# Kernel optimization log

Measured on AMD Instinct MI355X. Metric: run time of the kernel, lower is better.

## Reference

```python
import jax, jax.numpy as jnp
import numpy as np

B_, L, DM = 4, 1024, 1024
DI, DS, DR, DC = 1024, 16, 64, 4
NH = 4
DK = DM // NH


def setup_inputs() -> dict:
    key = jax.random.key(0)
    ks = jax.random.split(key, 16)
    def w(i, shape, scale=0.02):
        return jax.random.normal(ks[i], shape, dtype=jnp.float32) * scale
    inp = {
        "x": jax.random.normal(ks[0], (B_, L, DM), dtype=jnp.float32),
        "xx": jax.random.normal(ks[1], (B_, L, DI), dtype=jnp.float32),
        "in_proj_w": w(2, (DI, DM)),
        "conv_w": w(3, (DI, 1, DC)),            # depthwise conv, groups=DI
        "conv_b": jnp.zeros((DI,), jnp.float32),
        "x_proj_w": w(4, (DR + 2 * DS, DI)),
        "dt_proj_w": w(5, (DI, DR)),
        "dt_proj_b": jnp.zeros((DI,), jnp.float32),
        "A_log": jnp.log(jnp.tile(jnp.arange(1, DS + 1, dtype=jnp.float32)[None, :], (DI, 1))),
        "D": jnp.ones((DI,), jnp.float32),
        "wq": w(6, (DM, DM)), "bq": jnp.zeros((DM,), jnp.float32),
        "wk": w(7, (DM, DM)), "bk": jnp.zeros((DM,), jnp.float32),
        "wv": w(8, (DM, DM)), "bv": jnp.zeros((DM,), jnp.float32),
        "wo": w(9, (DM, DM)), "bo": jnp.zeros((DM,), jnp.float32),
    }
    return inp


def _stim_forward(x, xx, in_proj_w, conv_w, conv_b, x_proj_w, dt_proj_w, dt_proj_b,
                  A_log, D, wq, bq, wk, bk, wv, bv, wo, bo):
    b, l, _ = xx.shape
    # query branch: in_proj (Linear, no bias)
    q = x @ in_proj_w.T                                    # (b, l, DI)
    # kv branch: causal depthwise conv1d (padding d_conv-1, truncated to l)
    xc = jnp.transpose(xx, (0, 2, 1))                      # (b, DI, l)
    xc = jax.lax.conv_general_dilated(
        xc, conv_w, window_strides=(1,), padding=[(DC - 1, 0)],
        dimension_numbers=("NCH", "OIH", "NCH"), feature_group_count=DI)
    xc = xc + conv_b[None, :, None]
    u = jax.nn.silu(jnp.transpose(xc, (0, 2, 1)))          # (b, l, DI)
    # SSM parameter projections
    A = -jnp.exp(A_log)                                    # (DI, DS)
    x_dbl = u @ x_proj_w.T                                 # (b, l, DR+2*DS)
    delta, Bm, Cm = jnp.split(x_dbl, [DR, DR + DS], axis=-1)
    delta = jax.nn.softplus(delta @ dt_proj_w.T + dt_proj_b)  # (b, l, DI)
    deltaA = jnp.exp(jnp.einsum("bld,dn->bldn", delta, A))    # (b, l, DI, DS)
    deltaBu = jnp.einsum("bld,bln,bld->bldn", delta, Bm, u)   # (b, l, DI, DS)
    # selective scan over time
    def step(h, inp):
        dA_t, dBu_t, C_t = inp
        h = dA_t * h + dBu_t                               # (b, DI, DS)
        y_t = jnp.einsum("bdn,bn->bd", h, C_t)             # (b, DI)
        return h, y_t
    h0 = jnp.zeros((b, DI, DS), dtype=u.dtype)
    _, ys = jax.lax.scan(step, h0, (jnp.moveaxis(deltaA, 1, 0),
                                    jnp.moveaxis(deltaBu, 1, 0),
                                    jnp.moveaxis(Cm, 1, 0)))
    y = jnp.moveaxis(ys, 0, 1) + u * D                     # (b, l, DI)
    # cross attention: query = q, key/value = y
    Q = (q @ wq.T + bq).reshape(b, l, NH, DK).transpose(0, 2, 1, 3)
    K = (y @ wk.T + bk).reshape(b, l, NH, DK).transpose(0, 2, 1, 3)
    V = (y @ wv.T + bv).reshape(b, l, NH, DK).transpose(0, 2, 1, 3)
    scale = 1.0 / np.sqrt(DK).astype(np.float32)
    scores = jnp.einsum("bhqd,bhkd->bhqk", Q, K) * scale
    attn = jax.nn.softmax(scores, axis=-1)
    out = jnp.einsum("bhqk,bhkd->bhqd", attn, V)
    out = out.transpose(0, 2, 1, 3).reshape(b, l, DM)
    return out @ wo.T + bo


def reference(x, xx, in_proj_w, conv_w, conv_b, x_proj_w, dt_proj_w, dt_proj_b,
              A_log, D, wq, bq, wk, bk, wv, bv, wo, bo):
    return _stim_forward(x, xx, in_proj_w, conv_w, conv_b, x_proj_w, dt_proj_w,
                         dt_proj_b, A_log, D, wq, bq, wk, bk, wv, bv, wo, bo)
```

## Files before the change

kernel.cpp:

```cpp
#include <hip/hip_runtime.h>
#include <math.h>

#define B_  4
#define L_  1024
#define DM  1024
#define DI  1024
#define DS  16
#define DR  64
#define DCV 4
#define NH  4
#define DK  256

#define NCH 32
#define CHL (L_ / NCH)

typedef __attribute__((ext_vector_type(8))) short short8;
typedef __attribute__((ext_vector_type(4))) float floatx4;

static __device__ __forceinline__ unsigned short f2bf(float f) {
    unsigned int u = __float_as_uint(f);
    u += 0x7fffu + ((u >> 16) & 1u);
    return (unsigned short)(u >> 16);
}
static __device__ __forceinline__ float bf2f(unsigned short s) {
    return __uint_as_float(((unsigned int)s) << 16);
}

struct CastArgs {
    const float* s[8];
    unsigned short* d[8];
    int n[8];
    int ns[8];
};

__global__ __launch_bounds__(256) void cast_multi(CastArgs ca)
{
    int y = blockIdx.y;
    int i = (blockIdx.x * 256 + threadIdx.x) * 4;
    if (i >= ca.n[y]) return;
    const float* s = ca.s[y];
    unsigned short* d = ca.d[y];
    int ns = ca.ns[y];
    ushort4 o;
    if (i + 4 <= ns) {
        float4 v = *(const float4*)(s + i);
        o.x = f2bf(v.x); o.y = f2bf(v.y); o.z = f2bf(v.z); o.w = f2bf(v.w);
    } else {
        float v[4];
#pragma unroll
        for (int j = 0; j < 4; j++) v[j] = (i + j < ns) ? s[i + j] : 0.f;
        o.x = f2bf(v[0]); o.y = f2bf(v[1]); o.z = f2bf(v[2]); o.w = f2bf(v[3]);
    }
    *(ushort4*)(d + i) = o;
}

struct GDesc {
    const unsigned short* A;
    const unsigned short* W;
    const float* bias;
    float* Cf;
    unsigned short* Cb;
    int K, lda, ldw, ldc, ldc2;
    int mode;
    float scale;
    int gx, gy;
};
struct GArgs { GDesc g[3]; };

__global__ __launch_bounds__(256) void gemm_multi(GArgs ga)
{
    GDesc g = ga.g[blockIdx.z];
    if ((int)blockIdx.x >= g.gx || (int)blockIdx.y >= g.gy) return;

    __shared__ __align__(16) unsigned short Asm[128 * 32];
    __shared__ __align__(16) unsigned short Bsm[128 * 32];

    int tid = threadIdx.x;
    int wid = tid >> 6;
    int lane = tid & 63;
    int wm = wid & 1, wn = wid >> 1;
    int lr = lane & 15, quad = lane >> 4;

    const unsigned short* Ab = g.A + (size_t)blockIdx.y * 128 * g.lda;
    const unsigned short* Wb = g.W + (size_t)blockIdx.x * 128 * g.ldw;

    int srow = tid >> 2;
    int scol = (tid & 3) * 8;
    const unsigned short* Ap = Ab + (size_t)srow * g.lda + scol;
    const unsigned short* Wp = Wb + (size_t)srow * g.ldw + scol;

    unsigned short* lA0 = &Asm[(wid * 16) * 32];
    unsigned short* lA1 = &Asm[(64 + wid * 16) * 32];
    unsigned short* lB0 = &Bsm[(wid * 16) * 32];
    unsigned short* lB1 = &Bsm[(64 + wid * 16) * 32];

    floatx4 acc[4][4];
#pragma unroll
    for (int i = 0; i < 4; i++)
#pragma unroll
        for (int j = 0; j < 4; j++) acc[i][j] = (floatx4){0.f, 0.f, 0.f, 0.f};

#define GLL(gp, lp) __builtin_amdgcn_global_load_lds( \
        (const __attribute__((address_space(1))) void*)(gp), \
        (__attribute__((address_space(3))) void*)(lp), 16, 0, 0)

    for (int k0 = 0; k0 < g.K; k0 += 32) {
        GLL(Ap, lA0);
        GLL(Ap + (size_t)64 * g.lda, lA1);
        GLL(Wp, lB0);
        GLL(Wp + (size_t)64 * g.ldw, lB1);
        Ap += 32; Wp += 32;
        __syncthreads();

        short8 af[4], bf[4];
#pragma unroll
        for (int mt = 0; mt < 4; mt++)
            af[mt] = *(const short8*)&Asm[(wm * 64 + mt * 16 + lr) * 32 + quad * 8];
#pragma unroll
        for (int nt = 0; nt < 4; nt++)
            bf[nt] = *(const short8*)&Bsm[(wn * 64 + nt * 16 + lr) * 32 + quad * 8];
#pragma unroll
        for (int mt = 0; mt < 4; mt++)
#pragma unroll
            for (int nt = 0; nt < 4; nt++)
                acc[mt][nt] = __builtin_amdgcn_mfma_f32_16x16x32_bf16(
                    af[mt], bf[nt], acc[mt][nt], 0, 0, 0);
        __syncthreads();
    }
#undef GLL

    int bm = blockIdx.y * 128, bn = blockIdx.x * 128;
    int m = g.mode & 3;
#pragma unroll
    for (int mt = 0; mt < 4; mt++) {
#pragma unroll
        for (int nt = 0; nt < 4; nt++) {
            int row0 = bm + wm * 64 + mt * 16 + quad * 4;
            int col = bn + wn * 64 + nt * 16 + lr;
            float bv = g.bias ? g.bias[col] : 0.f;
#pragma unroll
            for (int i = 0; i < 4; i++) {
                float v = acc[mt][nt][i] * g.scale + bv;
                if (g.mode & 4) v = (v > 15.f) ? v : log1pf(__expf(v));
                if (m == 0) {
                    g.Cf[(size_t)(row0 + i) * g.ldc + col] = v;
                } else if (m == 1) {
                    g.Cb[(size_t)(row0 + i) * g.ldc + col] = f2bf(v);
                } else {
                    g.Cf[(size_t)(row0 + i) * g.ldc + col] = v;
                    g.Cb[(size_t)(row0 + i) * g.ldc2 + col] = f2bf(v);
                }
            }
        }
    }
}

__global__ __launch_bounds__(256) void flash_attn(
    const unsigned short* __restrict__ Q, const unsigned short* __restrict__ Kg,
    const unsigned short* __restrict__ VT, unsigned short* __restrict__ O)
{
    __shared__ __align__(16) unsigned short Ks[64 * 264];
    __shared__ __align__(16) unsigned short Pp[4 * 16 * 72];

    int bh = blockIdx.y;
    int b = bh >> 2, h = bh & 3;
    int q0 = blockIdx.x * 64;
    int tid = threadIdx.x;
    int wid = tid >> 6, lane = tid & 63;
    int lr = lane & 15, quad = lane >> 4;
    const float scale = 0.0625f;

    short8 qf[8];
    const unsigned short* qbase = Q + ((size_t)(b * L_ + q0 + wid * 16 + lr)) * 1024 + h * DK;
#pragma unroll
    for (int kf = 0; kf < 8; kf++)
        qf[kf] = *(const short8*)(qbase + kf * 32 + quad * 8);

    floatx4 o_acc[16];
#pragma unroll
    for (int i = 0; i < 16; i++) o_acc[i] = (floatx4){0.f, 0.f, 0.f, 0.f};
    float m_i[4] = {-3e38f, -3e38f, -3e38f, -3e38f};
    float l_i[4] = {0.f, 0.f, 0.f, 0.f};

    int srow = tid >> 5;
    int sc16 = tid & 31;
    unsigned short* pw = &Pp[wid * 16 * 72];

    for (int kt = 0; kt < 16; kt++) {
        int k0 = kt * 64;
        __syncthreads();
        {
            const unsigned short* kb = Kg + ((size_t)(b * L_ + k0 + srow)) * 1024 + h * DK + sc16 * 8;
            unsigned short* kd = &Ks[srow * 264 + sc16 * 8];
#pragma unroll
            for (int rd = 0; rd < 8; rd++)
                *(short8*)(kd + rd * 8 * 264) = *(const short8*)(kb + (size_t)rd * 8 * 1024);
        }
        __syncthreads();

        floatx4 sacc[4];
#pragma unroll
        for (int nt = 0; nt < 4; nt++) sacc[nt] = (floatx4){0.f, 0.f, 0.f, 0.f};
#pragma unroll
        for (int kf = 0; kf < 8; kf++) {
#pragma unroll
            for (int nt = 0; nt < 4; nt++) {
                short8 kfr = *(const short8*)&Ks[(nt * 16 + lr) * 264 + kf * 32 + quad * 8];
                sacc[nt] = __builtin_amdgcn_mfma_f32_16x16x32_bf16(qf[kf], kfr, sacc[nt], 0, 0, 0);
            }
        }

        float p_[4][4];
        float al[4];
#pragma unroll
        for (int i = 0; i < 4; i++) {
            float tm = sacc[0][i];
            tm = fmaxf(tm, sacc[1][i]);
            tm = fmaxf(tm, sacc[2][i]);
            tm = fmaxf(tm, sacc[3][i]);
            tm *= scale;
            tm = fmaxf(tm, __shfl_xor(tm, 1));
            tm = fmaxf(tm, __shfl_xor(tm, 2));
            tm = fmaxf(tm, __shfl_xor(tm, 4));
            tm = fmaxf(tm, __shfl_xor(tm, 8));
            float mn = fmaxf(m_i[i], tm);
            al[i] = __expf(m_i[i] - mn);
            m_i[i] = mn;
            float ts = 0.f;
#pragma unroll
            for (int nt = 0; nt < 4; nt++) {
                float pv = __expf(sacc[nt][i] * scale - mn);
                p_[nt][i] = pv;
                ts += pv;
            }
            ts += __shfl_xor(ts, 1);
            ts += __shfl_xor(ts, 2);
            ts += __shfl_xor(ts, 4);
            ts += __shfl_xor(ts, 8);
            l_i[i] = al[i] * l_i[i] + ts;
        }

#pragma unroll
        for (int nt = 0; nt < 4; nt++)
#pragma unroll
            for (int i = 0; i < 4; i++)
                pw[(quad * 4 + i) * 72 + nt * 16 + lr] = f2bf(p_[nt][i]);

#pragma unroll
        for (int ntd = 0; ntd < 16; ntd++) {
            floatx4 t = o_acc[ntd];
            t[0] *= al[0]; t[1] *= al[1]; t[2] *= al[2]; t[3] *= al[3];
            o_acc[ntd] = t;
        }

        const unsigned short* vb = VT + ((size_t)bh * DK + lr) * 1024 + k0 + quad * 8;
#pragma unroll
        for (int ko = 0; ko < 2; ko++) {
            short8 pf = *(const short8*)&pw[lr * 72 + ko * 32 + quad * 8];
#pragma unroll
            for (int ntd = 0; ntd < 16; ntd++) {
                short8 vf = *(const short8*)(vb + (size_t)ntd * 16 * 1024 + ko * 32);
                o_acc[ntd] = __builtin_amdgcn_mfma_f32_16x16x32_bf16(pf, vf, o_acc[ntd], 0, 0, 0);
            }
        }
    }

    float inv[4];
#pragma unroll
    for (int i = 0; i < 4; i++) inv[i] = 1.0f / l_i[i];
    unsigned short* ob = O + ((size_t)(b * L_ + q0 + wid * 16 + quad * 4)) * 1024 + h * DK + lr;
#pragma unroll
    for (int ntd = 0; ntd < 16; ntd++)
#pragma unroll
        for (int i = 0; i < 4; i++)
            ob[(size_t)i * 1024 + ntd * 16] = f2bf(o_acc[ntd][i] * inv[i]);
}

__global__ __launch_bounds__(256) void conv_silu_kernel(
    const float* __restrict__ xx, const float* __restrict__ cw,
    const float* __restrict__ cb, float* __restrict__ u,
    unsigned short* __restrict__ ub)
{
    int idx = blockIdx.x * 256 + threadIdx.x;
    int d = idx & (DI - 1);
    int l = (idx >> 10) & (L_ - 1);
    int b = idx >> 20;
    const float* xb = xx + (size_t)b * L_ * DI + d;
    float z = cb[d];
#pragma unroll
    for (int j = 0; j < DCV; j++) {
        int t = l - (DCV - 1) + j;
        if (t >= 0) z += xb[(size_t)t * DI] * cw[d * DCV + j];
    }
    float v = z / (1.0f + __expf(-z));
    u[idx] = v;
    ub[idx] = f2bf(v);
}

__global__ __launch_bounds__(256) void scan_a(
    const float* __restrict__ delta, const float* __restrict__ u,
    const float* __restrict__ xdbl, const float* __restrict__ A_log,
    float* __restrict__ Hc, float* __restrict__ sumdv)
{
    int gid = blockIdx.x * 256 + threadIdx.x;
    int c = gid >> 12;
    int bd = gid & 4095;
    int b = bd >> 10, d = bd & 1023;

    float a[16];
#pragma unroll
    for (int j = 0; j < 4; j++) {
        float4 al = *(const float4*)(A_log + d * 16 + j * 4);
        a[j * 4 + 0] = -__expf(al.x); a[j * 4 + 1] = -__expf(al.y);
        a[j * 4 + 2] = -__expf(al.z); a[j * 4 + 3] = -__expf(al.w);
    }
    float h[16];
#pragma unroll
    for (int n = 0; n < 16; n++) h[n] = 0.f;
    float sd = 0.f;

    int t0 = c * CHL;
    const float* dp = delta + ((size_t)(b * L_) + t0) * DI + d;
    const float* up = u + ((size_t)(b * L_) + t0) * DI + d;
    const float* xp = xdbl + ((size_t)(b * L_) + t0) * 128;

#pragma unroll 4
    for (int t = 0; t < CHL; t++) {
        float dv = dp[t * DI];
        float uv = up[t * DI];
        float duv = dv * uv;
        sd += dv;
        float Bv[16];
#pragma unroll
        for (int j = 0; j < 4; j++) {
            float4 bq = *(const float4*)(xp + t * 128 + 64 + j * 4);
            Bv[j * 4 + 0] = bq.x; Bv[j * 4 + 1] = bq.y;
            Bv[j * 4 + 2] = bq.z; Bv[j * 4 + 3] = bq.w;
        }
#pragma unroll
        for (int n = 0; n < 16; n++)
            h[n] = __expf(dv * a[n]) * h[n] + duv * Bv[n];
    }

    float* hp = Hc + ((size_t)c * 4096 + bd) * 16;
#pragma unroll
    for (int j = 0; j < 4; j++)
        *(float4*)(hp + j * 4) = make_float4(h[j * 4], h[j * 4 + 1], h[j * 4 + 2], h[j * 4 + 3]);
    sumdv[c * 4096 + bd] = sd;
}

__global__ __launch_bounds__(256) void scan_b(
    float* __restrict__ Hc, const float* __restrict__ sumdv,
    const float* __restrict__ A_log)
{
    int bd = blockIdx.x * 256 + threadIdx.x;
    int d = bd & 1023;

    float a[16];
#pragma unroll
    for (int j = 0; j < 4; j++) {
        float4 al = *(const float4*)(A_log + d * 16 + j * 4);
        a[j * 4 + 0] = -__expf(al.x); a[j * 4 + 1] = -__expf(al.y);
        a[j * 4 + 2] = -__expf(al.z); a[j * 4 + 3] = -__expf(al.w);
    }
    float H[16];
#pragma unroll
    for (int n = 0; n < 16; n++) H[n] = 0.f;

    for (int c = 0; c < NCH; c++) {
        float* hp = Hc + ((size_t)c * 4096 + bd) * 16;
        float sdv = sumdv[c * 4096 + bd];
        float hc[16];
#pragma unroll
        for (int j = 0; j < 4; j++) {
            float4 q = *(const float4*)(hp + j * 4);
            hc[j * 4 + 0] = q.x; hc[j * 4 + 1] = q.y; hc[j * 4 + 2] = q.z; hc[j * 4 + 3] = q.w;
        }
#pragma unroll
        for (int j = 0; j < 4; j++)
            *(float4*)(hp + j * 4) = make_float4(H[j * 4], H[j * 4 + 1], H[j * 4 + 2], H[j * 4 + 3]);
#pragma unroll
        for (int n = 0; n < 16; n++)
            H[n] = __expf(a[n] * sdv) * H[n] + hc[n];
    }
}

__global__ __launch_bounds__(256) void scan_c(
    const float* __restrict__ delta, const float* __restrict__ u,
    const float* __restrict__ xdbl, const float* __restrict__ A_log,
    const float* __restrict__ Dv, const float* __restrict__ Hstart,
    unsigned short* __restrict__ y)
{
    int gid = blockIdx.x * 256 + threadIdx.x;
    int c = gid >> 12;
    int bd = gid & 4095;
    int b = bd >> 10, d = bd & 1023;

    float a[16];
#pragma unroll
    for (int j = 0; j < 4; j++) {
        float4 al = *(const float4*)(A_log + d * 16 + j * 4);
        a[j * 4 + 0] = -__expf(al.x); a[j * 4 + 1] = -__expf(al.y);
        a[j * 4 + 2] = -__expf(al.z); a[j * 4 + 3] = -__expf(al.w);
    }
    float h[16];
    const float* hp = Hstart + ((size_t)c * 4096 + bd) * 16;
#pragma unroll
    for (int j = 0; j < 4; j++) {
        float4 q = *(const float4*)(hp + j * 4);
        h[j * 4 + 0] = q.x; h[j * 4 + 1] = q.y; h[j * 4 + 2] = q.z; h[j * 4 + 3] = q.w;
    }
    float Dd = Dv[d];

    int t0 = c * CHL;
    const float* dp = delta + ((size_t)(b * L_) + t0) * DI + d;
    const float* up = u + ((size_t)(b * L_) + t0) * DI + d;
    const float* xp = xdbl + ((size_t)(b * L_) + t0) * 128;
    unsigned short* yp = y + ((size_t)(b * L_) + t0) * DI + d;

#pragma unroll 4
    for (int t = 0; t < CHL; t++) {
        float dv = dp[t * DI];
        float uv = up[t * DI];
        float duv = dv * uv;
        float Bv[16], Cv[16];
#pragma unroll
        for (int j = 0; j < 4; j++) {
            float4 bq = *(const float4*)(xp + t * 128 + 64 + j * 4);
            Bv[j * 4 + 0] = bq.x; Bv[j * 4 + 1] = bq.y;
            Bv[j * 4 + 2] = bq.z; Bv[j * 4 + 3] = bq.w;
            float4 cq = *(const float4*)(xp + t * 128 + 80 + j * 4);
            Cv[j * 4 + 0] = cq.x; Cv[j * 4 + 1] = cq.y;
            Cv[j * 4 + 2] = cq.z; Cv[j * 4 + 3] = cq.w;
        }
        float ys = 0.f;
#pragma unroll
        for (int n = 0; n < 16; n++) {
            h[n] = __expf(dv * a[n]) * h[n] + duv * Bv[n];
            ys += h[n] * Cv[n];
        }
        yp[t * DI] = f2bf(ys + uv * Dd);
    }
}

__global__ __launch_bounds__(256) void transpose_v(
    const unsigned short* __restrict__ V, unsigned short* __restrict__ VT)
{
    __shared__ unsigned short tl[32][36];
    int bh = blockIdx.z;
    int b = bh >> 2, h = bh & 3;
    int l0 = blockIdx.x * 32, d0 = blockIdx.y * 32;
    int tid = threadIdx.x;
    int r = tid >> 3, c4 = (tid & 7) * 4;

    const unsigned short* src = V + ((size_t)(b * L_ + l0 + r)) * 1024 + h * DK + d0 + c4;
    ushort4 v = *(const ushort4*)src;
    tl[r][c4 + 0] = v.x; tl[r][c4 + 1] = v.y; tl[r][c4 + 2] = v.z; tl[r][c4 + 3] = v.w;
    __syncthreads();

    unsigned short* dst = VT + ((size_t)bh * DK + d0 + r) * L_ + l0 + c4;
    ushort4 o;
    o.x = tl[c4 + 0][r]; o.y = tl[c4 + 1][r]; o.z = tl[c4 + 2][r]; o.w = tl[c4 + 3][r];
    *(ushort4*)dst = o;
}

extern "C" void kernel_launch(void* const* d_in, const int* in_sizes, int n_in,
                              void* d_out, int out_size, void* d_ws, size_t ws_size,
                              hipStream_t stream)
{
    const float* x         = (const float*)d_in[0];
    const float* xx        = (const float*)d_in[1];
    const float* in_proj_w = (const float*)d_in[2];
    const float* conv_w    = (const float*)d_in[3];
    const float* conv_b    = (const float*)d_in[4];
    const float* x_proj_w  = (const float*)d_in[5];
    const float* dt_proj_w = (const float*)d_in[6];
    const float* dt_proj_b = (const float*)d_in[7];
    const float* A_log     = (const float*)d_in[8];
    const float* Dvec      = (const float*)d_in[9];
    const float* wq        = (const float*)d_in[10];
    const float* bq        = (const float*)d_in[11];
    const float* wk        = (const float*)d_in[12];
    const float* bk        = (const float*)d_in[13];
    const float* wv        = (const float*)d_in[14];
    const float* bv        = (const float*)d_in[15];
    const float* wo        = (const float*)d_in[16];
    const float* bo        = (const float*)d_in[17];
    float* out = (float*)d_out;

    char* w = (char*)d_ws;
    const size_t MB = 1024 * 1024, KB = 1024;
    float*          u_f    = (float*)(w + 0);
    float*          delta  = (float*)(w + 16 * MB);
    unsigned short* x_bf   = (unsigned short*)(w + 32 * MB);
    unsigned short* Q_bf   = x_bf;
    unsigned short* q_bf   = (unsigned short*)(w + 40 * MB);
    unsigned short* VT     = q_bf;
    unsigned short* y_bf   = (unsigned short*)(w + 48 * MB);
    unsigned short* AO     = y_bf;
    unsigned short* K_bf   = (unsigned short*)(w + 56 * MB);
    unsigned short* V_bf   = (unsigned short*)(w + 64 * MB);
    unsigned short* u_bf   = (unsigned short*)(w + 72 * MB);
    float*          Hc     = (float*)(w + 72 * MB);
    float*          xdbl   = (float*)(w + 80 * MB);
    unsigned short* xdblb  = (unsigned short*)(w + 82 * MB);
    unsigned short* w_in   = (unsigned short*)(w + 83 * MB);
    unsigned short* w_q    = (unsigned short*)(w + 85 * MB);
    unsigned short* w_k    = (unsigned short*)(w + 87 * MB);
    unsigned short* w_v    = (unsigned short*)(w + 89 * MB);
    unsigned short* w_o    = (unsigned short*)(w + 91 * MB);
    unsigned short* w_xp   = (unsigned short*)(w + 93 * MB);
    unsigned short* w_dt   = (unsigned short*)(w + 93 * MB + 256 * KB);
    float*          sumdv  = (float*)(w + 93 * MB + 384 * KB);

    dim3 blk(256);

    CastArgs ca;
    ca.s[0] = x;         ca.d[0] = x_bf;  ca.n[0] = 4194304; ca.ns[0] = 4194304;
    ca.s[1] = in_proj_w; ca.d[1] = w_in;  ca.n[1] = 1048576; ca.ns[1] = 1048576;
    ca.s[2] = wq;        ca.d[2] = w_q;   ca.n[2] = 1048576; ca.ns[2] = 1048576;
    ca.s[3] = wk;        ca.d[3] = w_k;   ca.n[3] = 1048576; ca.ns[3] = 1048576;
    ca.s[4] = wv;        ca.d[4] = w_v;   ca.n[4] = 1048576; ca.ns[4] = 1048576;
    ca.s[5] = wo;        ca.d[5] = w_o;   ca.n[5] = 1048576; ca.ns[5] = 1048576;
    ca.s[6] = x_proj_w;  ca.d[6] = w_xp;  ca.n[6] = 131072;  ca.ns[6] = 98304;
    ca.s[7] = dt_proj_w; ca.d[7] = w_dt;  ca.n[7] = 65536;   ca.ns[7] = 65536;
    cast_multi<<<dim3(4096, 8), blk, 0, stream>>>(ca);

    conv_silu_kernel<<<dim3(16384), blk, 0, stream>>>(xx, conv_w, conv_b, u_f, u_bf);

    {
        GArgs ga = {};
        ga.g[0] = (GDesc){x_bf, w_in, nullptr, nullptr, q_bf,
                          1024, 1024, 1024, 1024, 0, 1, 1.0f, 8, 32};
        ga.g[1] = (GDesc){u_bf, w_xp, nullptr, xdbl, xdblb,
                          1024, 1024, 1024, 128, 128, 2, 1.0f, 1, 32};
        gemm_multi<<<dim3(8, 32, 2), blk, 0, stream>>>(ga);
    }
    {
        GArgs ga = {};
        ga.g[0] = (GDesc){xdblb, w_dt, dt_proj_b, delta, nullptr,
                          64, 128, 64, 1024, 0, 0 | 4, 1.0f, 8, 32};
        gemm_multi<<<dim3(8, 32, 1), blk, 0, stream>>>(ga);
    }
    scan_a<<<dim3(512), blk, 0, stream>>>(delta, u_f, xdbl, A_log, Hc, sumdv);
    scan_b<<<dim3(16), blk, 0, stream>>>(Hc, sumdv, A_log);
    scan_c<<<dim3(512), blk, 0, stream>>>(delta, u_f, xdbl, A_log, Dvec, Hc, y_bf);

    {
        GArgs ga = {};
        ga.g[0] = (GDesc){q_bf, w_q, bq, nullptr, Q_bf, 1024, 1024, 1024, 1024, 0, 1, 1.0f, 8, 32};
        ga.g[1] = (GDesc){y_bf, w_k, bk, nullptr, K_bf, 1024, 1024, 1024, 1024, 0, 1, 1.0f, 8, 32};
        ga.g[2] = (GDesc){y_bf, w_v, bv, nullptr, V_bf, 1024, 1024, 1024, 1024, 0, 1, 1.0f, 8, 32};
        gemm_multi<<<dim3(8, 32, 3), blk, 0, stream>>>(ga);
    }
    transpose_v<<<dim3(32, 8, 16), blk, 0, stream>>>(V_bf, VT);
    flash_attn<<<dim3(16, 16), blk, 0, stream>>>(Q_bf, K_bf, VT, AO);
    {
        GArgs ga = {};
        ga.g[0] = (GDesc){AO, w_o, bo, out, nullptr, 1024, 1024, 1024, 1024, 0, 0, 1.0f, 8, 32};
        gemm_multi<<<dim3(8, 32, 1), blk, 0, stream>>>(ga);
    }
}
```

Baseline: 479.4 us.

## Use direct global-to-LDS K loads and register-prefetched V in flash attention

The flash attention kernel now fills shared memory with K tiles through global_load_lds in an MFMA-fragment-friendly layout. The next K tile is loaded at the end of each iteration. V fragments are loaded into registers early so their latency overlaps the QK MFMAs and the softmax. The grid is flattened so consecutive blocks cover different heads, and launch bounds request one block per CU. The aim is to hide memory latency in attention, at the cost of more register pressure from the 32 prefetched V vectors.

```diff
diff --git a/kernel.cpp b/kernel.cpp
--- a/kernel.cpp
+++ b/kernel.cpp
@@ -155,16 +155,18 @@
     }
 }
 
-__global__ __launch_bounds__(256) void flash_attn(
+__global__ __launch_bounds__(256, 1) void flash_attn(
     const unsigned short* __restrict__ Q, const unsigned short* __restrict__ Kg,
     const unsigned short* __restrict__ VT, unsigned short* __restrict__ O)
 {
-    __shared__ __align__(16) unsigned short Ks[64 * 264];
+    __shared__ __align__(16) unsigned short Ks[32 * 512];
     __shared__ __align__(16) unsigned short Pp[4 * 16 * 72];
 
-    int bh = blockIdx.y;
+    int id = blockIdx.x;
+    int bh = id & 15;
+    int qt = id >> 4;
     int b = bh >> 2, h = bh & 3;
-    int q0 = blockIdx.x * 64;
+    int q0 = qt * 64;
     int tid = threadIdx.x;
     int wid = tid >> 6, lane = tid & 63;
     int lr = lane & 15, quad = lane >> 4;
@@ -182,21 +184,32 @@
     float m_i[4] = {-3e38f, -3e38f, -3e38f, -3e38f};
     float l_i[4] = {0.f, 0.f, 0.f, 0.f};
 
-    int srow = tid >> 5;
-    int sc16 = tid & 31;
     unsigned short* pw = &Pp[wid * 16 * 72];
+
+    {
+#pragma unroll
+        for (int j = 0; j < 8; j++) {
+            int f = wid * 8 + j;
+            int nt_ = f & 3, kf_ = f >> 2;
+            const unsigned short* gp = Kg + ((size_t)(b * L_ + nt_ * 16 + lr)) * 1024
+                                       + h * DK + kf_ * 32 + quad * 8;
+            __builtin_amdgcn_global_load_lds(
+                (const __attribute__((address_space(1))) void*)gp,
+                (__attribute__((address_space(3))) void*)(&Ks[(kf_ * 4 + nt_) * 512]),
+                16, 0, 0);
+        }
+    }
+    __syncthreads();
+
+    const unsigned short* vbase = VT + ((size_t)bh * DK + lr) * 1024 + quad * 8;
 
     for (int kt = 0; kt < 16; kt++) {
         int k0 = kt * 64;
-        __syncthreads();
-        {
-            const unsigned short* kb = Kg + ((size_t)(b * L_ + k0 + srow)) * 1024 + h * DK + sc16 * 8;
-            unsigned short* kd = &Ks[srow * 264 + sc16 * 8];
-#pragma unroll
-            for (int rd = 0; rd < 8; rd++)
-                *(short8*)(kd + rd * 8 * 264) = *(const short8*)(kb + (size_t)rd * 8 * 1024);
-        }
-        __syncthreads();
+
+        short8 vf0[16], vf1[16];
+#pragma unroll
+        for (int ntd = 0; ntd < 16; ntd++)
+            vf0[ntd] = *(const short8*)(vbase + (size_t)ntd * 16 * 1024 + k0);
 
         floatx4 sacc[4];
 #pragma unroll
@@ -205,10 +218,14 @@
         for (int kf = 0; kf < 8; kf++) {
 #pragma unroll
             for (int nt = 0; nt < 4; nt++) {
-                short8 kfr = *(const short8*)&Ks[(nt * 16 + lr) * 264 + kf * 32 + quad * 8];
+                short8 kfr = *(const short8*)&Ks[(kf * 4 + nt) * 512 + lane * 8];
                 sacc[nt] = __builtin_amdgcn_mfma_f32_16x16x32_bf16(qf[kf], kfr, sacc[nt], 0, 0, 0);
             }
         }
+
+#pragma unroll
+        for (int ntd = 0; ntd < 16; ntd++)
+            vf1[ntd] = *(const short8*)(vbase + (size_t)ntd * 16 * 1024 + k0 + 32);
 
         float p_[4][4];
         float al[4];
@@ -253,16 +270,31 @@
             o_acc[ntd] = t;
         }
 
-        const unsigned short* vb = VT + ((size_t)bh * DK + lr) * 1024 + k0 + quad * 8;
-#pragma unroll
-        for (int ko = 0; ko < 2; ko++) {
-            short8 pf = *(const short8*)&pw[lr * 72 + ko * 32 + quad * 8];
-#pragma unroll
-            for (int ntd = 0; ntd < 16; ntd++) {
-                short8 vf = *(const short8*)(vb + (size_t)ntd * 16 * 1024 + ko * 32);
-                o_acc[ntd] = __builtin_amdgcn_mfma_f32_16x16x32_bf16(pf, vf, o_acc[ntd], 0, 0, 0);
+        short8 pf0 = *(const short8*)&pw[lr * 72 + quad * 8];
+        short8 pf1 = *(const short8*)&pw[lr * 72 + 32 + quad * 8];
+#pragma unroll
+        for (int ntd = 0; ntd < 16; ntd++)
+            o_acc[ntd] = __builtin_amdgcn_mfma_f32_16x16x32_bf16(pf0, vf0[ntd], o_acc[ntd], 0, 0, 0);
+#pragma unroll
+        for (int ntd = 0; ntd < 16; ntd++)
+            o_acc[ntd] = __builtin_amdgcn_mfma_f32_16x16x32_bf16(pf1, vf1[ntd], o_acc[ntd], 0, 0, 0);
+
+        __syncthreads();
+        if (kt < 15) {
+            int kn = k0 + 64;
+#pragma unroll
+            for (int j = 0; j < 8; j++) {
+                int f = wid * 8 + j;
+                int nt_ = f & 3, kf_ = f >> 2;
+                const unsigned short* gp = Kg + ((size_t)(b * L_ + kn + nt_ * 16 + lr)) * 1024
+                                           + h * DK + kf_ * 32 + quad * 8;
+                __builtin_amdgcn_global_load_lds(
+                    (const __attribute__((address_space(1))) void*)gp,
+                    (__attribute__((address_space(3))) void*)(&Ks[(kf_ * 4 + nt_) * 512]),
+                    16, 0, 0);
             }
         }
+        __syncthreads();
     }
 
     float inv[4];
@@ -554,7 +586,7 @@
         gemm_multi<<<dim3(8, 32, 3), blk, 0, stream>>>(ga);
     }
     transpose_v<<<dim3(32, 8, 16), blk, 0, stream>>>(V_bf, VT);
-    flash_attn<<<dim3(16, 16), blk, 0, stream>>>(Q_bf, K_bf, VT, AO);
+    flash_attn<<<dim3(256), blk, 0, stream>>>(Q_bf, K_bf, VT, AO);
     {
         GArgs ga = {};
         ga.g[0] = (GDesc){AO, w_o, bo, out, nullptr, 1024, 1024, 1024, 1024, 0, 0, 1.0f, 8, 32};
```

Result: faster. 469.8 us (-2.0%).

## Split attention over key range with partial outputs and merge kernel

Applied to the files above, without the earlier changes.

Flash attention now splits the 1024 keys into two halves, launching 512 blocks instead of 256 so more of the GPU's compute units get work. Each block writes unnormalised fp32 partial outputs plus running max and sum, and a new merge kernel rescales and combines them into bf16. K is read straight from global memory instead of being staged in LDS, and V fragments are preloaded into registers before the score computation. The cost is an extra kernel launch, fp32 partial-output traffic through the workspace, and possibly more register pressure from the V preloads under the tighter launch bounds.

```diff
diff --git a/kernel.cpp b/kernel.cpp
--- a/kernel.cpp
+++ b/kernel.cpp
@@ -155,16 +155,19 @@
     }
 }
 
-__global__ __launch_bounds__(256) void flash_attn(
+__global__ __launch_bounds__(256, 2) void flash_attn(
     const unsigned short* __restrict__ Q, const unsigned short* __restrict__ Kg,
-    const unsigned short* __restrict__ VT, unsigned short* __restrict__ O)
-{
-    __shared__ __align__(16) unsigned short Ks[64 * 264];
+    const unsigned short* __restrict__ VT, float* __restrict__ Opart,
+    float* __restrict__ mbuf, float* __restrict__ lbuf)
+{
     __shared__ __align__(16) unsigned short Pp[4 * 16 * 72];
 
-    int bh = blockIdx.y;
+    int id = blockIdx.x;
+    int bh = id & 15;
+    int qt = (id >> 4) & 15;
+    int sk = id >> 8;
     int b = bh >> 2, h = bh & 3;
-    int q0 = blockIdx.x * 64;
+    int q0 = qt * 64;
     int tid = threadIdx.x;
     int wid = tid >> 6, lane = tid & 63;
     int lr = lane & 15, quad = lane >> 4;
@@ -182,21 +185,17 @@
     float m_i[4] = {-3e38f, -3e38f, -3e38f, -3e38f};
     float l_i[4] = {0.f, 0.f, 0.f, 0.f};
 
-    int srow = tid >> 5;
-    int sc16 = tid & 31;
     unsigned short* pw = &Pp[wid * 16 * 72];
-
-    for (int kt = 0; kt < 16; kt++) {
-        int k0 = kt * 64;
-        __syncthreads();
-        {
-            const unsigned short* kb = Kg + ((size_t)(b * L_ + k0 + srow)) * 1024 + h * DK + sc16 * 8;
-            unsigned short* kd = &Ks[srow * 264 + sc16 * 8];
-#pragma unroll
-            for (int rd = 0; rd < 8; rd++)
-                *(short8*)(kd + rd * 8 * 264) = *(const short8*)(kb + (size_t)rd * 8 * 1024);
-        }
-        __syncthreads();
+    const unsigned short* vbase = VT + ((size_t)bh * DK + lr) * 1024 + quad * 8;
+    const unsigned short* kbase = Kg + ((size_t)(b * L_) + lr) * 1024 + h * DK + quad * 8;
+
+    for (int kt = 0; kt < 8; kt++) {
+        int k0 = sk * 512 + kt * 64;
+
+        short8 vf[16];
+#pragma unroll
+        for (int ntd = 0; ntd < 16; ntd++)
+            vf[ntd] = *(const short8*)(vbase + (size_t)ntd * 16 * 1024 + k0);
 
         floatx4 sacc[4];
 #pragma unroll
@@ -205,7 +204,7 @@
         for (int kf = 0; kf < 8; kf++) {
 #pragma unroll
             for (int nt = 0; nt < 4; nt++) {
-                short8 kfr = *(const short8*)&Ks[(nt * 16 + lr) * 264 + kf * 32 + quad * 8];
+                short8 kfr = *(const short8*)(kbase + (size_t)(k0 + nt * 16) * 1024 + kf * 32);
                 sacc[nt] = __builtin_amdgcn_mfma_f32_16x16x32_bf16(qf[kf], kfr, sacc[nt], 0, 0, 0);
             }
         }
@@ -253,27 +252,65 @@
             o_acc[ntd] = t;
         }
 
-        const unsigned short* vb = VT + ((size_t)bh * DK + lr) * 1024 + k0 + quad * 8;
-#pragma unroll
-        for (int ko = 0; ko < 2; ko++) {
-            short8 pf = *(const short8*)&pw[lr * 72 + ko * 32 + quad * 8];
-#pragma unroll
-            for (int ntd = 0; ntd < 16; ntd++) {
-                short8 vf = *(const short8*)(vb + (size_t)ntd * 16 * 1024 + ko * 32);
-                o_acc[ntd] = __builtin_amdgcn_mfma_f32_16x16x32_bf16(pf, vf, o_acc[ntd], 0, 0, 0);
-            }
-        }
-    }
-
-    float inv[4];
-#pragma unroll
-    for (int i = 0; i < 4; i++) inv[i] = 1.0f / l_i[i];
-    unsigned short* ob = O + ((size_t)(b * L_ + q0 + wid * 16 + quad * 4)) * 1024 + h * DK + lr;
+        short8 pf0 = *(const short8*)&pw[lr * 72 + quad * 8];
+        short8 pf1 = *(const short8*)&pw[lr * 72 + 32 + quad * 8];
+
+#pragma unroll
+        for (int ntd = 0; ntd < 16; ntd++)
+            o_acc[ntd] = __builtin_amdgcn_mfma_f32_16x16x32_bf16(pf0, vf[ntd], o_acc[ntd], 0, 0, 0);
+
+#pragma unroll
+        for (int ntd = 0; ntd < 16; ntd++)
+            vf[ntd] = *(const short8*)(vbase + (size_t)ntd * 16 * 1024 + k0 + 32);
+#pragma unroll
+        for (int ntd = 0; ntd < 16; ntd++)
+            o_acc[ntd] = __builtin_amdgcn_mfma_f32_16x16x32_bf16(pf1, vf[ntd], o_acc[ntd], 0, 0, 0);
+    }
+
+    float* ob = Opart + (size_t)sk * 4194304
+              + ((size_t)(b * L_ + q0 + wid * 16 + quad * 4)) * 1024 + h * DK + lr;
 #pragma unroll
     for (int ntd = 0; ntd < 16; ntd++)
 #pragma unroll
         for (int i = 0; i < 4; i++)
-            ob[(size_t)i * 1024 + ntd * 16] = f2bf(o_acc[ntd][i] * inv[i]);
+            ob[(size_t)i * 1024 + ntd * 16] = o_acc[ntd][i];
+
+    if (lr == 0) {
+        int row = q0 + wid * 16 + quad * 4;
+#pragma unroll
+        for (int i = 0; i < 4; i++) {
+            mbuf[sk * 16384 + bh * 1024 + row + i] = m_i[i];
+            lbuf[sk * 16384 + bh * 1024 + row + i] = l_i[i];
+        }
+    }
+}
+
+__global__ __launch_bounds__(256) void attn_merge(
+    const float* __restrict__ Opart, const float* __restrict__ mbuf,
+    const float* __restrict__ lbuf, unsigned short* __restrict__ AO)
+{
+    int gid = blockIdx.x * 256 + threadIdx.x;
+    int row = gid >> 8;
+    int c4 = (gid & 255) * 4;
+    int b = row >> 10, l = row & 1023;
+    int bh = b * 4 + (c4 >> 8);
+    int mo = bh * 1024 + l;
+
+    float m0 = mbuf[mo], l0 = lbuf[mo];
+    float m1 = mbuf[16384 + mo], l1 = lbuf[16384 + mo];
+    float M = fmaxf(m0, m1);
+    float w0 = __expf(m0 - M), w1 = __expf(m1 - M);
+    float inv = 1.0f / (w0 * l0 + w1 * l1);
+
+    size_t o = (size_t)row * 1024 + c4;
+    float4 a0 = *(const float4*)(Opart + o);
+    float4 a1 = *(const float4*)(Opart + 4194304 + o);
+    ushort4 r;
+    r.x = f2bf((w0 * a0.x + w1 * a1.x) * inv);
+    r.y = f2bf((w0 * a0.y + w1 * a1.y) * inv);
+    r.z = f2bf((w0 * a0.z + w1 * a1.z) * inv);
+    r.w = f2bf((w0 * a0.w + w1 * a1.w) * inv);
+    *(ushort4*)(AO + o) = r;
 }
 
 __global__ __launch_bounds__(256) void conv_silu_kernel(
@@ -492,6 +529,7 @@
     const size_t MB = 1024 * 1024, KB = 1024;
     float*          u_f    = (float*)(w + 0);
     float*          delta  = (float*)(w + 16 * MB);
+    float*          Opart  = (float*)(w + 0);
     unsigned short* x_bf   = (unsigned short*)(w + 32 * MB);
     unsigned short* Q_bf   = x_bf;
     unsigned short* q_bf   = (unsigned short*)(w + 40 * MB);
@@ -512,6 +550,8 @@
     unsigned short* w_xp   = (unsigned short*)(w + 93 * MB);
     unsigned short* w_dt   = (unsigned short*)(w + 93 * MB + 256 * KB);
     float*          sumdv  = (float*)(w + 93 * MB + 384 * KB);
+    float*          mbuf   = (float*)(w + 94 * MB);
+    float*          lbuf   = (float*)(w + 94 * MB + 256 * KB);
 
     dim3 blk(256);
 
@@ -554,7 +594,8 @@
         gemm_multi<<<dim3(8, 32, 3), blk, 0, stream>>>(ga);
     }
     transpose_v<<<dim3(32, 8, 16), blk, 0, stream>>>(V_bf, VT);
-    flash_attn<<<dim3(16, 16), blk, 0, stream>>>(Q_bf, K_bf, VT, AO);
+    flash_attn<<<dim3(512), blk, 0, stream>>>(Q_bf, K_bf, VT, Opart, mbuf, lbuf);
+    attn_merge<<<dim3(4096), blk, 0, stream>>>(Opart, mbuf, lbuf, AO);
     {
         GArgs ga = {};
         ga.g[0] = (GDesc){AO, w_o, bo, out, nullptr, 1024, 1024, 1024, 1024, 0, 0, 1.0f, 8, 32};
```

New measurement: 507.2 us. 5.8% more time.
